# Optimization experiments

Measured on AMD Instinct MI355X. Metric: run time of the kernel, lower is better.

## Reference

```python
import jax, jax.numpy as jnp
import numpy as np

B, T = 4096, 2048
C_MCC, C_TR = 100, 50
EPS = 1e-9


def setup_inputs() -> dict:
    key = jax.random.key(0)
    k1, k2, k3, k4 = jax.random.split(key, 4)
    amount = jax.random.normal(k1, (B, T), dtype=jnp.float32)
    # category 0 is the padding token, masked out by (1 - ohe[0]); draw from [1, C)
    mcc = jax.random.randint(k2, (B, T), 1, C_MCC, dtype=jnp.int32)
    tr_type = jax.random.randint(k3, (B, T), 1, C_TR, dtype=jnp.int32)
    seq_lens = jax.random.randint(k4, (B,), 1, T + 1, dtype=jnp.int32)
    return {"amount": amount, "mcc": mcc, "tr_type": tr_type, "seq_lens": seq_lens}


def _cat_aggs(cat, val, C):
    """Per-(batch,category) count / mean / std of val, via scatter-add.
    Equivalent to the torch one-hot-matmul formulation but without the
    [B,T,C] one-hot intermediate."""
    Bb, Tt = cat.shape
    flat = (jnp.arange(Bb)[:, None] * C + cat).reshape(-1)  # [B*T]
    z = jnp.zeros(Bb * C, dtype=val.dtype)
    cnt = z.at[flat].add(1.0).reshape(Bb, C)                 # ohe.sum(dim=1)
    s = z.at[flat].add(val.reshape(-1)).reshape(Bb, C)       # (ohe*val).sum(dim=1)
    ss = z.at[flat].add((val * val).reshape(-1)).reshape(Bb, C)
    mask = (jnp.arange(C) > 0).astype(val.dtype)[None, :]    # 1 - ohe[0]
    e_cnt = cnt * mask
    e_mean = s / (e_cnt + EPS)
    a = jnp.clip(ss - s * s / (e_cnt + EPS), 0.0)
    e_std = jnp.sqrt(a / (jnp.clip(e_cnt - 1.0, 0.0) + EPS))
    return e_cnt, e_mean, e_std


def _forward(amount, mcc, tr_type, seq_lens):
    sl = seq_lens.astype(amount.dtype)
    processed = [sl[:, None]]
    # numeric column aggregates (was_logified=False path)
    s = amount.sum(axis=1)
    mean_ = s / (sl + EPS)
    a = jnp.clip((amount * amount).sum(axis=1) - s * s / (sl + EPS), 0.0)
    std_ = jnp.sqrt(a / (jnp.clip(sl - 1.0, 0.0) + EPS))
    processed += [s[:, None], mean_[:, None], std_[:, None]]
    distinct = []
    for cat, C in ((mcc, C_MCC), (tr_type, C_TR)):
        e_cnt, e_mean, e_std = _cat_aggs(cat, amount, C)
        processed += [e_cnt, e_mean, e_std]
        # e_cnt.gt(0).float().sum(dim=1, keepdim=True)
        distinct.append((e_cnt > 0.0).astype(amount.dtype).sum(axis=1, keepdims=True))
    return jnp.concatenate(processed + distinct, axis=1)  # [B, 456]


def reference(amount, mcc, tr_type, seq_lens):
    return _forward(amount, mcc, tr_type, seq_lens)
```

## Files before the change

kernel.cpp:

```cpp
#include <hip/hip_runtime.h>
#include <stdint.h>


#define NCOL 456
static constexpr float EPS = 1e-9f;

typedef __bf16 bf16x8 __attribute__((ext_vector_type(8)));
typedef float  f32x4  __attribute__((ext_vector_type(4)));
typedef int    i32x8  __attribute__((ext_vector_type(8)));
typedef unsigned int u32x4 __attribute__((ext_vector_type(4)));
typedef short  s16x2  __attribute__((ext_vector_type(2)));

__device__ __forceinline__ uint32_t hw_eqmask(uint32_t h) {
    const uint32_t s = 0x80008000u - h;
    const s16x2 m = __builtin_bit_cast(s16x2, s) >> 15;
    return __builtin_bit_cast(uint32_t, m);
}

__device__ __forceinline__ uint32_t pack_lobytes(int4 m) {
    const uint32_t p01 = __builtin_amdgcn_perm((uint32_t)m.y, (uint32_t)m.x, 0x00000400u);
    const uint32_t p23 = __builtin_amdgcn_perm((uint32_t)m.w, (uint32_t)m.z, 0x00000400u);
    return __builtin_amdgcn_perm(p23, p01, 0x05040100u);
}

#define WSTR 784
#define MOFF 256
#define TOFF 528

__global__ __launch_bounds__(64, 4) void agg_fused(
    const float4* __restrict__ a4,
    const int4* __restrict__ m4,
    const int4* __restrict__ t4,
    const int* __restrict__ seq_lens,
    float* __restrict__ out, int B)
{
    const int lane = threadIdx.x;
    const int row  = blockIdx.x;
    const int n    = lane & 15;
    const int grp  = lane >> 4;
    const bool istr = (grp >= 2);
    const int ntc  = istr ? ((n - 7) & 15) : n;
    const uint32_t patB = (uint32_t)(((ntc << 4) | n) * 0x01010101u);

    __shared__ uint32_t ws[WSTR];

    f32x4 accC = {0.f,0.f,0.f,0.f};
    f32x4 accS = {0.f,0.f,0.f,0.f};
    f32x4 accQ = {0.f,0.f,0.f,0.f};
    float s_p = 0.f, q_p = 0.f;

    const uint8_t* pv = (const uint8_t*)ws + ((grp & 1) << 5);
    const uint8_t* pk = (const uint8_t*)(ws + (istr ? TOFF : MOFF)) + ((grp & 1) << 5);

#pragma unroll 1
    for (int h = 0; h < 2; ++h) {
        const size_t g4 = (size_t)row * 512 + h * 256;
#pragma unroll
        for (int j = 0; j < 4; ++j) {
            const size_t gi = g4 + j * 64 + lane;
            const float4 a = a4[gi];
            const int4   m = m4[gi];
            const int4   t = t4[gi];
            uint32_t w = __builtin_amdgcn_cvt_pk_fp8_f32(a.x, a.y, 0u, false);
            w = __builtin_amdgcn_cvt_pk_fp8_f32(a.z, a.w, w, true);
            ws[j * 64 + lane]        = w;
            ws[MOFF + j * 64 + lane] = pack_lobytes(m);
            ws[TOFF + j * 64 + lane] = pack_lobytes(t);
            s_p += (a.x + a.y) + (a.z + a.w);
            q_p = fmaf(a.x, a.x, fmaf(a.y, a.y, fmaf(a.z, a.z, fmaf(a.w, a.w, q_p))));
        }

#pragma unroll 2
        for (int st = 0; st < 16; ++st) {
            const int off = st << 6;
            const uint4 v0 = *reinterpret_cast<const uint4*>(pv + off);
            const uint4 v1 = *reinterpret_cast<const uint4*>(pv + off + 16);
            const uint4 k0 = *reinterpret_cast<const uint4*>(pk + off);
            const uint4 k1 = *reinterpret_cast<const uint4*>(pk + off + 16);

            i32x8 fA1, fAa, fB1, fBa;
#define DOW(j, kw, vw) { \
            const uint32_t kx = (kw) ^ patB; \
            const uint32_t hu = kx & 0x0f0f0f0fu; \
            const uint32_t mu = (((0x80808080u - hu) & 0x80808080u) >> 7) * 255u; \
            const uint32_t ht = (kx >> 4) & 0x0f0f0f0fu; \
            const uint32_t mt = (((0x80808080u - ht) & 0x80808080u) >> 7) * 255u; \
            fA1[j] = (int)(mt & 0x38383838u);   \
            fAa[j] = (int)(mt & (vw)); \
            fB1[j] = (int)(mu & 0x38383838u); \
            fBa[j] = (int)(mu & (vw)); }
            DOW(0, k0.x, v0.x) DOW(1, k0.y, v0.y) DOW(2, k0.z, v0.z) DOW(3, k0.w, v0.w)
            DOW(4, k1.x, v1.x) DOW(5, k1.y, v1.y) DOW(6, k1.z, v1.z) DOW(7, k1.w, v1.w)
#undef DOW

            accC = __builtin_amdgcn_mfma_scale_f32_16x16x128_f8f6f4(
                       fA1, fB1, accC, 0, 0, 0, 0x7f7f7f7f, 0, 0x7f7f7f7f);
            accS = __builtin_amdgcn_mfma_scale_f32_16x16x128_f8f6f4(
                       fA1, fBa, accS, 0, 0, 0, 0x7f7f7f7f, 0, 0x7f7f7f7f);
            accQ = __builtin_amdgcn_mfma_scale_f32_16x16x128_f8f6f4(
                       fAa, fBa, accQ, 0, 0, 0, 0x7f7f7f7f, 0, 0x7f7f7f7f);
        }
    }

    float* tbl = (float*)ws;
#pragma unroll
    for (int r = 0; r < 4; ++r) {
        const int rr = grp * 4 + r;
        int addr = -1;
        if (rr <= 6)       addr = rr * 16 + n;
        else if (rr <= 10) addr = 112 + (rr - 7) * 16 + n;
        if (addr >= 0) {
            tbl[addr]       = accC[r];
            tbl[176 + addr] = accS[r];
            tbl[352 + addr] = accQ[r];
        }
    }
    asm volatile("s_waitcnt lgkmcnt(0)" ::: "memory");
    __builtin_amdgcn_sched_barrier(0);

    int dm = 0, dt = 0;
    for (int c0 = 0; c0 < 160; c0 += 64) {
        const int c = c0 + lane;
        bool pos = false;
        if (c >= 1 && c < 100)        pos = tbl[c] > 0.f;
        else if (c >= 101 && c < 150) pos = tbl[112 + (c - 100)] > 0.f;
        dm += __popcll(__ballot(pos && c < 100));
        dt += __popcll(__ballot(pos && c >= 100));
    }

#pragma unroll
    for (int off = 32; off; off >>= 1) {
        s_p += __shfl_xor(s_p, off, 64);
        q_p += __shfl_xor(q_p, off, 64);
    }
    const float s_tot = s_p, ss_tot = q_p;
    const float sl = (float)seq_lens[row];
    float* orow = out + (size_t)row * NCOL;

    for (int cc = lane; cc < NCOL; cc += 64) {
        const int col = cc;
        float v;
        if (col == 0)      v = sl;
        else if (col == 1) v = s_tot;
        else if (col == 2) v = s_tot / (sl + EPS);
        else if (col == 3) {
            float a = fmaxf(ss_tot - s_tot * s_tot / (sl + EPS), 0.f);
            v = sqrtf(a / (fmaxf(sl - 1.f, 0.f) + EPS));
        }
        else if (col == 454) v = (float)dm;
        else if (col == 455) v = (float)dt;
        else {
            int base, C, toff;
            if (col < 304) { base = 4;   C = 100; toff = 0;   }
            else           { base = 304; C = 50;  toff = 112; }
            const int rel   = col - base;
            const int which = rel / C;
            const int c     = rel - which * C;
            const float cnt = (c > 0) ? tbl[toff + c] : 0.f;
            const float sc  = tbl[176 + toff + c];
            const float ssc = tbl[352 + toff + c];
            if (which == 0)      v = cnt;
            else if (which == 1) v = sc / (cnt + EPS);
            else {
                float a = fmaxf(ssc - sc * sc / (cnt + EPS), 0.f);
                v = sqrtf(a / (fmaxf(cnt - 1.f, 0.f) + EPS));
            }
        }
        orow[col] = v;
    }
}

__global__ __launch_bounds__(512, 8) void agg2d_legacy(
    const float* __restrict__ amount,
    const int* __restrict__ mcc,
    const int* __restrict__ tr,
    const int* __restrict__ seq_lens,
    float* __restrict__ out, int T, int B)
{
    const int lane = threadIdx.x & 63;
    const int wv   = threadIdx.x >> 6;
    const int rl   = wv >> 1;
    const int half = wv & 1;
    const int row  = blockIdx.x * 4 + rl;
    const int n    = lane & 15;
    const int grp  = lane >> 4;
    const bool istr = (grp >= 2);
    const int ntc  = istr ? ((n - 7) & 15) : n;
    const uint32_t xorpat = (uint32_t)(((ntc << 4) | n) * 0x00010001u);
    const int roff = (grp & 1) * 8;

    __shared__ float part[4][2][3][176];
    __shared__ float scal[4][2][2];

    const int hb = half * (T >> 1);
    const float* pa = amount + (size_t)row * T + hb + roff;
    const int*   pk = (istr ? tr : mcc) + (size_t)row * T + hb + roff;

    f32x4 accC = {0.f,0.f,0.f,0.f};
    f32x4 accS = {0.f,0.f,0.f,0.f};
    f32x4 accQ = {0.f,0.f,0.f,0.f};

    const int nstep = T >> 5;
#pragma unroll 2
    for (int st = 0; st < nstep; ++st) {
        const int base = st << 4;
        const float4 a0 = *reinterpret_cast<const float4*>(pa + base);
        const float4 a1 = *reinterpret_cast<const float4*>(pa + base + 4);
        const int4   k0 = *reinterpret_cast<const int4*>(pk + base);
        const int4   k1 = *reinterpret_cast<const int4*>(pk + base + 4);

        const float av[8] = {a0.x,a0.y,a0.z,a0.w,a1.x,a1.y,a1.z,a1.w};
        const uint32_t kv[8] = {(uint32_t)k0.x,(uint32_t)k0.y,(uint32_t)k0.z,(uint32_t)k0.w,
                                (uint32_t)k1.x,(uint32_t)k1.y,(uint32_t)k1.z,(uint32_t)k1.w};

        u32x4 wA1, wAa, wB1, wBa;
#pragma unroll
        for (int i = 0; i < 4; ++i) {
            const uint32_t kpk = __builtin_amdgcn_perm(kv[2*i+1], kv[2*i], 0x05040100u);
            const uint32_t kx  = kpk ^ xorpat;
            const uint32_t mu  = hw_eqmask(kx & 0x000f000fu);
            const uint32_t mt  = hw_eqmask((kx >> 4) & 0x000f000fu);
            const uint32_t apk = __builtin_amdgcn_perm(
                __float_as_uint(av[2*i+1]), __float_as_uint(av[2*i]), 0x07060302u);
            wA1[i] = mt & 0x3f803f80u;
            wAa[i] = mt & apk;
            wB1[i] = mu & 0x3f803f80u;
            wBa[i] = mu & apk;
        }
        const bf16x8 fA1 = __builtin_bit_cast(bf16x8, wA1);
        const bf16x8 fAa = __builtin_bit_cast(bf16x8, wAa);
        const bf16x8 fB1 = __builtin_bit_cast(bf16x8, wB1);
        const bf16x8 fBa = __builtin_bit_cast(bf16x8, wBa);

        accC = __builtin_amdgcn_mfma_f32_16x16x32_bf16(fA1, fB1, accC, 0, 0, 0);
        accS = __builtin_amdgcn_mfma_f32_16x16x32_bf16(fA1, fBa, accS, 0, 0, 0);
        accQ = __builtin_amdgcn_mfma_f32_16x16x32_bf16(fAa, fBa, accQ, 0, 0, 0);
    }

    {
        float* my = &part[rl][half][0][0];
#pragma unroll
        for (int r = 0; r < 4; ++r) {
            const int rr = grp * 4 + r;
            int addr = -1;
            if (rr <= 6)       addr = rr * 16 + n;
            else if (rr <= 10) addr = 112 + (rr - 7) * 16 + n;
            if (addr >= 0) {
                my[addr]       = accC[r];
                my[176 + addr] = accS[r];
                my[352 + addr] = accQ[r];
            }
        }
    }
    float sS = 0.f, sQ = 0.f;
    if (grp == 0) {
        sS = accS[0] + accS[1] + accS[2] + accS[3];
        sQ = accQ[0] + accQ[1] + accQ[2] + accQ[3];
    } else if (grp == 1) {
        sS = accS[0] + accS[1] + accS[2];
        sQ = accQ[0] + accQ[1] + accQ[2];
    }
#pragma unroll
    for (int off = 32; off; off >>= 1) {
        sS += __shfl_xor(sS, off, 64);
        sQ += __shfl_xor(sQ, off, 64);
    }
    if (lane == 0) { scal[rl][half][0] = sS; scal[rl][half][1] = sQ; }
    __syncthreads();

    auto TB = [&](int s, int c) -> float {
        return part[rl][0][s][c] + part[rl][1][s][c];
    };

    int dm = 0, dt = 0;
    if (half) {
        for (int c0 = 0; c0 < 160; c0 += 64) {
            const int c = c0 + lane;
            bool pos = false;
            if (c >= 1 && c < 100)        pos = TB(0, c) > 0.f;
            else if (c >= 101 && c < 150) pos = TB(0, 112 + (c - 100)) > 0.f;
            dm += __popcll(__ballot(pos && c < 100));
            dt += __popcll(__ballot(pos && c >= 100));
        }
    }

    const float sl     = (float)seq_lens[row];
    const float s_tot  = scal[rl][0][0] + scal[rl][1][0];
    const float ss_tot = scal[rl][0][1] + scal[rl][1][1];
    float* orow = out + (size_t)row * NCOL;

    for (int cc = lane; cc < 228; cc += 64) {
        const int col = half * 228 + cc;
        float v;
        if (col == 0)      v = sl;
        else if (col == 1) v = s_tot;
        else if (col == 2) v = s_tot / (sl + EPS);
        else if (col == 3) {
            float a = fmaxf(ss_tot - s_tot * s_tot / (sl + EPS), 0.f);
            v = sqrtf(a / (fmaxf(sl - 1.f, 0.f) + EPS));
        }
        else if (col == 454) v = (float)dm;
        else if (col == 455) v = (float)dt;
        else {
            int base, C, toff;
            if (col < 304) { base = 4;   C = 100; toff = 0;   }
            else           { base = 304; C = 50;  toff = 112; }
            const int rel   = col - base;
            const int which = rel / C;
            const int c     = rel - which * C;
            const float cnt = (c > 0) ? TB(0, toff + c) : 0.f;
            const float sc  = TB(1, toff + c);
            const float ssc = TB(2, toff + c);
            if (which == 0)      v = cnt;
            else if (which == 1) v = sc / (cnt + EPS);
            else {
                float a = fmaxf(ssc - sc * sc / (cnt + EPS), 0.f);
                v = sqrtf(a / (fmaxf(cnt - 1.f, 0.f) + EPS));
            }
        }
        orow[col] = v;
    }
}

extern "C" void kernel_launch(void* const* d_in, const int* in_sizes, int n_in,
                              void* d_out, int out_size, void* d_ws, size_t ws_size,
                              hipStream_t stream) {
    const float* amount   = (const float*)d_in[0];
    const int*   mcc      = (const int*)d_in[1];
    const int*   tr_type  = (const int*)d_in[2];
    const int*   seq_lens = (const int*)d_in[3];
    float*       out      = (float*)d_out;

    const int B = in_sizes[3];
    const int T = in_sizes[0] / B;

    if (T == 2048) {
        agg_fused<<<B, 64, 0, stream>>>(
            (const float4*)amount, (const int4*)mcc, (const int4*)tr_type,
            seq_lens, out, B);
    } else {
        agg2d_legacy<<<(B + 3) / 4, 512, 0, stream>>>(amount, mcc, tr_type, seq_lens, out, T, B);
    }
}
```

Baseline: 46.49 us.

## Split each row's two halves across two wavefronts and merge via shared memory

Each block now runs two wavefronts instead of one. Each wave processes half of the row's 2048 elements into its own shared-memory tile and MFMA accumulators. The per-category tables from both waves are summed when read, the scalar sums are combined through a small shared array after a block barrier, and the output columns are split between the waves. This doubles parallelism per row and removes the serial two-pass loop, at the cost of doubled shared memory per block, an added __syncthreads, and extra reads during the final merge.

```diff
diff --git a/kernel.cpp b/kernel.cpp
--- a/kernel.cpp
+++ b/kernel.cpp
@@ -27,14 +27,15 @@
 #define MOFF 256
 #define TOFF 528
 
-__global__ __launch_bounds__(64, 4) void agg_fused(
+__global__ __launch_bounds__(128, 4) void agg_fused(
     const float4* __restrict__ a4,
     const int4* __restrict__ m4,
     const int4* __restrict__ t4,
     const int* __restrict__ seq_lens,
     float* __restrict__ out, int B)
 {
-    const int lane = threadIdx.x;
+    const int lane = threadIdx.x & 63;
+    const int wv   = threadIdx.x >> 6;
     const int row  = blockIdx.x;
     const int n    = lane & 15;
     const int grp  = lane >> 4;
@@ -42,7 +43,9 @@
     const int ntc  = istr ? ((n - 7) & 15) : n;
     const uint32_t patB = (uint32_t)(((ntc << 4) | n) * 0x01010101u);
 
-    __shared__ uint32_t ws[WSTR];
+    __shared__ uint32_t smem[2 * WSTR];
+    __shared__ float scal[2][2];
+    uint32_t* ws = smem + wv * WSTR;
 
     f32x4 accC = {0.f,0.f,0.f,0.f};
     f32x4 accS = {0.f,0.f,0.f,0.f};
@@ -52,93 +55,99 @@
     const uint8_t* pv = (const uint8_t*)ws + ((grp & 1) << 5);
     const uint8_t* pk = (const uint8_t*)(ws + (istr ? TOFF : MOFF)) + ((grp & 1) << 5);
 
-#pragma unroll 1
-    for (int h = 0; h < 2; ++h) {
-        const size_t g4 = (size_t)row * 512 + h * 256;
-#pragma unroll
-        for (int j = 0; j < 4; ++j) {
-            const size_t gi = g4 + j * 64 + lane;
-            const float4 a = a4[gi];
-            const int4   m = m4[gi];
-            const int4   t = t4[gi];
-            uint32_t w = __builtin_amdgcn_cvt_pk_fp8_f32(a.x, a.y, 0u, false);
-            w = __builtin_amdgcn_cvt_pk_fp8_f32(a.z, a.w, w, true);
-            ws[j * 64 + lane]        = w;
-            ws[MOFF + j * 64 + lane] = pack_lobytes(m);
-            ws[TOFF + j * 64 + lane] = pack_lobytes(t);
-            s_p += (a.x + a.y) + (a.z + a.w);
-            q_p = fmaf(a.x, a.x, fmaf(a.y, a.y, fmaf(a.z, a.z, fmaf(a.w, a.w, q_p))));
-        }
+    const size_t g4 = (size_t)row * 512 + wv * 256;
+#pragma unroll
+    for (int j = 0; j < 4; ++j) {
+        const size_t gi = g4 + j * 64 + lane;
+        const float4 a = a4[gi];
+        const int4   m = m4[gi];
+        const int4   t = t4[gi];
+        uint32_t w = __builtin_amdgcn_cvt_pk_fp8_f32(a.x, a.y, 0u, false);
+        w = __builtin_amdgcn_cvt_pk_fp8_f32(a.z, a.w, w, true);
+        ws[j * 64 + lane]        = w;
+        ws[MOFF + j * 64 + lane] = pack_lobytes(m);
+        ws[TOFF + j * 64 + lane] = pack_lobytes(t);
+        s_p += (a.x + a.y) + (a.z + a.w);
+        q_p = fmaf(a.x, a.x, fmaf(a.y, a.y, fmaf(a.z, a.z, fmaf(a.w, a.w, q_p))));
+    }
 
 #pragma unroll 2
-        for (int st = 0; st < 16; ++st) {
-            const int off = st << 6;
-            const uint4 v0 = *reinterpret_cast<const uint4*>(pv + off);
-            const uint4 v1 = *reinterpret_cast<const uint4*>(pv + off + 16);
-            const uint4 k0 = *reinterpret_cast<const uint4*>(pk + off);
-            const uint4 k1 = *reinterpret_cast<const uint4*>(pk + off + 16);
-
-            i32x8 fA1, fAa, fB1, fBa;
+    for (int st = 0; st < 16; ++st) {
+        const int off = st << 6;
+        const uint4 v0 = *reinterpret_cast<const uint4*>(pv + off);
+        const uint4 v1 = *reinterpret_cast<const uint4*>(pv + off + 16);
+        const uint4 k0 = *reinterpret_cast<const uint4*>(pk + off);
+        const uint4 k1 = *reinterpret_cast<const uint4*>(pk + off + 16);
+
+        i32x8 fA1, fAa, fB1, fBa;
 #define DOW(j, kw, vw) { \
-            const uint32_t kx = (kw) ^ patB; \
-            const uint32_t hu = kx & 0x0f0f0f0fu; \
-            const uint32_t mu = (((0x80808080u - hu) & 0x80808080u) >> 7) * 255u; \
-            const uint32_t ht = (kx >> 4) & 0x0f0f0f0fu; \
-            const uint32_t mt = (((0x80808080u - ht) & 0x80808080u) >> 7) * 255u; \
-            fA1[j] = (int)(mt & 0x38383838u);   \
-            fAa[j] = (int)(mt & (vw)); \
-            fB1[j] = (int)(mu & 0x38383838u); \
-            fBa[j] = (int)(mu & (vw)); }
-            DOW(0, k0.x, v0.x) DOW(1, k0.y, v0.y) DOW(2, k0.z, v0.z) DOW(3, k0.w, v0.w)
-            DOW(4, k1.x, v1.x) DOW(5, k1.y, v1.y) DOW(6, k1.z, v1.z) DOW(7, k1.w, v1.w)
+        const uint32_t kx = (kw) ^ patB; \
+        const uint32_t hu = kx & 0x0f0f0f0fu; \
+        const uint32_t mu = (((0x80808080u - hu) & 0x80808080u) >> 7) * 255u; \
+        const uint32_t ht = (kx >> 4) & 0x0f0f0f0fu; \
+        const uint32_t mt = (((0x80808080u - ht) & 0x80808080u) >> 7) * 255u; \
+        fA1[j] = (int)(mt & 0x38383838u);   \
+        fAa[j] = (int)(mt & (vw)); \
+        fB1[j] = (int)(mu & 0x38383838u); \
+        fBa[j] = (int)(mu & (vw)); }
+        DOW(0, k0.x, v0.x) DOW(1, k0.y, v0.y) DOW(2, k0.z, v0.z) DOW(3, k0.w, v0.w)
+        DOW(4, k1.x, v1.x) DOW(5, k1.y, v1.y) DOW(6, k1.z, v1.z) DOW(7, k1.w, v1.w)
 #undef DOW
 
-            accC = __builtin_amdgcn_mfma_scale_f32_16x16x128_f8f6f4(
-                       fA1, fB1, accC, 0, 0, 0, 0x7f7f7f7f, 0, 0x7f7f7f7f);
-            accS = __builtin_amdgcn_mfma_scale_f32_16x16x128_f8f6f4(
-                       fA1, fBa, accS, 0, 0, 0, 0x7f7f7f7f, 0, 0x7f7f7f7f);
-            accQ = __builtin_amdgcn_mfma_scale_f32_16x16x128_f8f6f4(
-                       fAa, fBa, accQ, 0, 0, 0, 0x7f7f7f7f, 0, 0x7f7f7f7f);
-        }
-    }
-
-    float* tbl = (float*)ws;
-#pragma unroll
-    for (int r = 0; r < 4; ++r) {
-        const int rr = grp * 4 + r;
-        int addr = -1;
-        if (rr <= 6)       addr = rr * 16 + n;
-        else if (rr <= 10) addr = 112 + (rr - 7) * 16 + n;
-        if (addr >= 0) {
-            tbl[addr]       = accC[r];
-            tbl[176 + addr] = accS[r];
-            tbl[352 + addr] = accQ[r];
-        }
-    }
-    asm volatile("s_waitcnt lgkmcnt(0)" ::: "memory");
-    __builtin_amdgcn_sched_barrier(0);
-
-    int dm = 0, dt = 0;
-    for (int c0 = 0; c0 < 160; c0 += 64) {
-        const int c = c0 + lane;
-        bool pos = false;
-        if (c >= 1 && c < 100)        pos = tbl[c] > 0.f;
-        else if (c >= 101 && c < 150) pos = tbl[112 + (c - 100)] > 0.f;
-        dm += __popcll(__ballot(pos && c < 100));
-        dt += __popcll(__ballot(pos && c >= 100));
-    }
-
+        accC = __builtin_amdgcn_mfma_scale_f32_16x16x128_f8f6f4(
+                   fA1, fB1, accC, 0, 0, 0, 0x7f7f7f7f, 0, 0x7f7f7f7f);
+        accS = __builtin_amdgcn_mfma_scale_f32_16x16x128_f8f6f4(
+                   fA1, fBa, accS, 0, 0, 0, 0x7f7f7f7f, 0, 0x7f7f7f7f);
+        accQ = __builtin_amdgcn_mfma_scale_f32_16x16x128_f8f6f4(
+                   fAa, fBa, accQ, 0, 0, 0, 0x7f7f7f7f, 0, 0x7f7f7f7f);
+    }
+
+    {
+        float* tbl = (float*)ws;
+#pragma unroll
+        for (int r = 0; r < 4; ++r) {
+            const int rr = grp * 4 + r;
+            int addr = -1;
+            if (rr <= 6)       addr = rr * 16 + n;
+            else if (rr <= 10) addr = 112 + (rr - 7) * 16 + n;
+            if (addr >= 0) {
+                tbl[addr]       = accC[r];
+                tbl[176 + addr] = accS[r];
+                tbl[352 + addr] = accQ[r];
+            }
+        }
+    }
 #pragma unroll
     for (int off = 32; off; off >>= 1) {
         s_p += __shfl_xor(s_p, off, 64);
         q_p += __shfl_xor(q_p, off, 64);
     }
-    const float s_tot = s_p, ss_tot = q_p;
+    if (lane == 0) { scal[wv][0] = s_p; scal[wv][1] = q_p; }
+    __syncthreads();
+
+    const float* t0 = (const float*)smem;
+    const float* t1 = (const float*)(smem + WSTR);
+    auto TB = [&](int s, int c) -> float { return t0[s * 176 + c] + t1[s * 176 + c]; };
+
+    int dm = 0, dt = 0;
+    if (wv) {
+        for (int c0 = 0; c0 < 160; c0 += 64) {
+            const int c = c0 + lane;
+            bool pos = false;
+            if (c >= 1 && c < 100)        pos = TB(0, c) > 0.f;
+            else if (c >= 101 && c < 150) pos = TB(0, 112 + (c - 100)) > 0.f;
+            dm += __popcll(__ballot(pos && c < 100));
+            dt += __popcll(__ballot(pos && c >= 100));
+        }
+    }
+
+    const float s_tot  = scal[0][0] + scal[1][0];
+    const float ss_tot = scal[0][1] + scal[1][1];
     const float sl = (float)seq_lens[row];
     float* orow = out + (size_t)row * NCOL;
 
-    for (int cc = lane; cc < NCOL; cc += 64) {
-        const int col = cc;
+    for (int cc = lane; cc < 228; cc += 64) {
+        const int col = wv * 228 + cc;
         float v;
         if (col == 0)      v = sl;
         else if (col == 1) v = s_tot;
@@ -156,9 +165,9 @@
             const int rel   = col - base;
             const int which = rel / C;
             const int c     = rel - which * C;
-            const float cnt = (c > 0) ? tbl[toff + c] : 0.f;
-            const float sc  = tbl[176 + toff + c];
-            const float ssc = tbl[352 + toff + c];
+            const float cnt = (c > 0) ? TB(0, toff + c) : 0.f;
+            const float sc  = TB(1, toff + c);
+            const float ssc = TB(2, toff + c);
             if (which == 0)      v = cnt;
             else if (which == 1) v = sc / (cnt + EPS);
             else {
@@ -335,7 +344,7 @@
     const int T = in_sizes[0] / B;
 
     if (T == 2048) {
-        agg_fused<<<B, 64, 0, stream>>>(
+        agg_fused<<<B, 128, 0, stream>>>(
             (const float4*)amount, (const int4*)mcc, (const int4*)tr_type,
             seq_lens, out, B);
     } else {
```

Result: no change. 45.93 us (-1.2%).
